# Kernel optimization log

Hardware: AMD Instinct MI355X
Metric: run time of the kernel (lower is better)

The kernel has to match this reference:

```python
import jax, jax.numpy as jnp
import numpy as np

B, LQ, C = 2, 12240, 256
NH, NL, NP = 8, 4, 4          # heads, levels, points
D = C // NH                   # head dim = 32
SHAPES = np.array([[96, 96], [48, 48], [24, 24], [12, 12]], dtype=np.int32)
LEN_IN = int((SHAPES[:, 0] * SHAPES[:, 1]).sum())  # 12240


def setup_inputs() -> dict:
    key = jax.random.key(0)
    ks = jax.random.split(key, 10)
    start = np.concatenate([[0], np.cumsum(SHAPES[:, 0] * SHAPES[:, 1])[:-1]]).astype(np.int32)
    return {
        "query": jax.random.normal(ks[0], (B, LQ, C), jnp.float32),
        "reference_points": jax.random.uniform(ks[1], (B, LQ, NL, 2), jnp.float32),
        "input_flatten": jax.random.normal(ks[2], (B, LEN_IN, C), jnp.float32),
        "input_spatial_shapes": jnp.asarray(SHAPES),
        "input_level_start_index": jnp.asarray(start),
        # params (sampling_offsets weight kept small so samples land near the reference point)
        "W_off": jax.random.normal(ks[3], (C, NH * NL * NP * 2), jnp.float32) * 0.01,
        "b_off": jax.random.normal(ks[4], (NH * NL * NP * 2,), jnp.float32) * 0.1,
        "W_attn": jax.random.normal(ks[5], (C, NH * NL * NP), jnp.float32) * 0.02,
        "b_attn": jnp.zeros((NH * NL * NP,), jnp.float32),
        "W_val": jax.random.normal(ks[6], (C, C), jnp.float32) * (1.0 / np.sqrt(C)),
        "b_val": jnp.zeros((C,), jnp.float32),
        "W_out": jax.random.normal(ks[7], (C, C), jnp.float32) * (1.0 / np.sqrt(C)),
        "b_out": jnp.zeros((C,), jnp.float32),
    }


def _bilinear_sample(v, loc):
    """grid_sample(align_corners=False, padding=zeros) equivalent.
    v:   (B, Hl, Wl, NH, D) level feature map per head
    loc: (B, Lq, NH, NP, 2) normalized sampling locations in [0,1]
    ->   (B, Lq, NH, NP, D)
    """
    _, Hl, Wl, _, _ = v.shape
    x = loc[..., 0] * Wl - 0.5
    y = loc[..., 1] * Hl - 0.5
    x0 = jnp.floor(x); y0 = jnp.floor(y)
    lx = x - x0;       ly = y - y0
    x0i = x0.astype(jnp.int32); y0i = y0.astype(jnp.int32)
    bi = jnp.arange(v.shape[0])[:, None, None, None]
    hi = jnp.arange(NH)[None, None, :, None]

    def gather(yi, xi):
        valid = (yi >= 0) & (yi < Hl) & (xi >= 0) & (xi < Wl)
        yc = jnp.clip(yi, 0, Hl - 1)
        xc = jnp.clip(xi, 0, Wl - 1)
        g = v[bi, yc, xc, hi]                       # (B,Lq,NH,NP,D)
        return g * valid[..., None].astype(v.dtype)

    w00 = (1 - lx) * (1 - ly); w01 = lx * (1 - ly)
    w10 = (1 - lx) * ly;       w11 = lx * ly
    return (gather(y0i, x0i) * w00[..., None] + gather(y0i, x0i + 1) * w01[..., None]
            + gather(y0i + 1, x0i) * w10[..., None] + gather(y0i + 1, x0i + 1) * w11[..., None])


def reference(query, reference_points, input_flatten, input_spatial_shapes,
              input_level_start_index, W_off, b_off, W_attn, b_attn,
              W_val, b_val, W_out, b_out):
    shapes = np.asarray(input_spatial_shapes)          # static level geometry
    starts = np.asarray(input_level_start_index)

    value = (input_flatten @ W_val + b_val).reshape(B, LEN_IN, NH, D)
    offsets = (query @ W_off + b_off).reshape(B, LQ, NH, NL, NP, 2)
    attn = (query @ W_attn + b_attn).reshape(B, LQ, NH, NL * NP)
    attn = jax.nn.softmax(attn, axis=-1).reshape(B, LQ, NH, NL, NP)

    # normalizer is (W_l, H_l) per level
    normalizer = jnp.stack([input_spatial_shapes[:, 1], input_spatial_shapes[:, 0]], -1).astype(query.dtype)
    loc = (reference_points[:, :, None, :, None, :]
           + offsets / normalizer[None, None, None, :, None, :])  # (B,Lq,NH,NL,NP,2)

    out = jnp.zeros((B, LQ, NH, D), query.dtype)
    for l in range(NL):
        Hl, Wl = int(shapes[l, 0]), int(shapes[l, 1])
        s = int(starts[l])
        v_l = value[:, s:s + Hl * Wl].reshape(B, Hl, Wl, NH, D)
        sampled = _bilinear_sample(v_l, loc[:, :, :, l])            # (B,Lq,NH,NP,D)
        out = out + jnp.einsum("bqhpd,bqhp->bqhd", sampled, attn[:, :, :, l])
    out = out.reshape(B, LQ, C)
    return out @ W_out + b_out
```

## Files before the change

### kernel.cpp

```cpp
#include <hip/hip_runtime.h>
#include <math.h>

#define B_    2
#define LQ_   12240
#define C_    256
#define NH_   8
#define NL_   4
#define NP_   4
#define LEN_IN_ 12240
#define MROWS (B_*LQ_)
#define MF_   (MROWS/16)
#define KF_   8
#define APLANE ((size_t)MROWS * C_)
#define NBLK  383

typedef __attribute__((ext_vector_type(8))) short short8v;
typedef __attribute__((ext_vector_type(4))) float f32x4;

__device__ __forceinline__ ushort f2bf_hi(float f) {
    uint u = __builtin_bit_cast(uint, f);
    uint r = (u + 0x7fffu + ((u >> 16) & 1u)) >> 16;
    return (ushort)r;
}
__device__ __forceinline__ float bf2f(ushort h) {
    uint u = ((uint)h) << 16;
    return __builtin_bit_cast(float, u);
}

#define U4_VAL  0
#define U4_OFF  8192
#define U4_ATT  16384
#define U4_UHI  20480
#define U4_ULO  28672
#define PACKB_TOTAL 294912

__global__ __launch_bounds__(256) void pack_w_kernel(
    const float* __restrict__ Wv, const float* __restrict__ Wo,
    const float* __restrict__ Wa, const float* __restrict__ Wu,
    ushort* __restrict__ packB)
{
    int gid = blockIdx.x * 256 + threadIdx.x;
    if (gid >= 28672) return;
    const float* W; ushort* hi; ushort* lo = nullptr; int N, rel;
    if (gid < 8192)       { W = Wv; hi = packB;          N = 256; rel = gid; }
    else if (gid < 16384) { W = Wo; hi = packB + 65536;  N = 256; rel = gid - 8192; }
    else if (gid < 20480) { W = Wa; hi = packB + 131072; N = 128; rel = gid - 16384; }
    else { W = Wu; hi = packB + 163840; lo = packB + 229376; N = 256; rel = gid - 20480; }

    const int lane = rel & 63;
    const int kf   = (rel >> 6) & 7;
    const int nf   = rel >> 9;
    const int row0 = kf * 32 + (lane >> 4) * 8;
    const int col  = nf * 16 + (lane & 15);

    union { ushort u16[8]; uint4 u4; } ch, cl;
#pragma unroll
    for (int j = 0; j < 8; ++j) {
        float x = W[(size_t)(row0 + j) * N + col];
        ushort h = f2bf_hi(x);
        ch.u16[j] = h;
        cl.u16[j] = f2bf_hi(x - bf2f(h));
    }
    *reinterpret_cast<uint4*>(hi + (size_t)rel * 8) = ch.u4;
    if (lo) *reinterpret_cast<uint4*>(lo + (size_t)rel * 8) = cl.u4;
}

__global__ __launch_bounds__(512) void gemm_value_kernel(
    const float* __restrict__ A, const ushort* __restrict__ packB,
    const float* __restrict__ bias, ushort* __restrict__ Cg)
{
    const int t = threadIdx.x, lane = t & 63, wid = t >> 6;
    const int rowBase = blockIdx.x * 64;

    __shared__ ushort Als[2048 * 8];

#pragma unroll
    for (int i = 0; i < 4; ++i) {
        int frag = i * 512 + t;
        int fl = frag & 63, kf = (frag >> 6) & 7, mf = frag >> 9;
        int row = min(rowBase + mf * 16 + (fl & 15), MROWS - 1);
        int k0 = kf * 32 + (fl >> 4) * 8;
        const float4* s = reinterpret_cast<const float4*>(A + (size_t)row * 256 + k0);
        float4 v0 = s[0], v1 = s[1];
        float vv[8] = { v0.x, v0.y, v0.z, v0.w, v1.x, v1.y, v1.z, v1.w };
        union { ushort u16[8]; uint4 u4; } hh;
#pragma unroll
        for (int j = 0; j < 8; ++j) hh.u16[j] = f2bf_hi(vv[j]);
        *reinterpret_cast<uint4*>(&Als[(size_t)frag * 8]) = hh.u4;
    }
    __syncthreads();

    const uint4* B4 = reinterpret_cast<const uint4*>(packB) + U4_VAL;
    const uint4* A4 = reinterpret_cast<const uint4*>(Als);
    const int wnf = wid * 2;

    f32x4 acc[4][2];
#pragma unroll
    for (int mi = 0; mi < 4; ++mi)
#pragma unroll
        for (int f = 0; f < 2; ++f) acc[mi][f] = (f32x4)0.0f;

#pragma unroll
    for (int kf = 0; kf < KF_; ++kf) {
        uint4 bh[2], ah[4];
#pragma unroll
        for (int f = 0; f < 2; ++f) bh[f] = B4[((wnf + f) * KF_ + kf) * 64 + lane];
#pragma unroll
        for (int mi = 0; mi < 4; ++mi) ah[mi] = A4[(mi * KF_ + kf) * 64 + lane];
#pragma unroll
        for (int mi = 0; mi < 4; ++mi) {
            short8v a = __builtin_bit_cast(short8v, ah[mi]);
#pragma unroll
            for (int f = 0; f < 2; ++f)
                acc[mi][f] = __builtin_amdgcn_mfma_f32_16x16x32_bf16(
                    a, __builtin_bit_cast(short8v, bh[f]), acc[mi][f], 0, 0, 0);
        }
    }

    const int colLane = lane & 15, rquad = lane >> 4;
#pragma unroll
    for (int f = 0; f < 2; ++f) {
        int col = (wnf + f) * 16 + colLane;
        float bv = bias[col];
#pragma unroll
        for (int mi = 0; mi < 4; ++mi)
#pragma unroll
            for (int e = 0; e < 4; ++e) {
                int row = rowBase + mi * 16 + rquad * 4 + e;
                if (row < MROWS) Cg[(size_t)row * 256 + col] = f2bf_hi(acc[mi][f][e] + bv);
            }
    }
}

__global__ __launch_bounds__(768) void gemm_query_kernel(
    const float* __restrict__ A, const ushort* __restrict__ packB,
    const float* __restrict__ b_off, const float* __restrict__ b_attn,
    float* __restrict__ offsb, float* __restrict__ attnb)
{
    const int t = threadIdx.x, lane = t & 63, wid = t >> 6;
    const int rowBase = blockIdx.x * 64;

    __shared__ ushort Als[2048 * 8];

#pragma unroll
    for (int i = 0; i < 3; ++i) {
        int frag = i * 768 + t;
        if (frag < 2048) {
            int fl = frag & 63, kf = (frag >> 6) & 7, mf = frag >> 9;
            int row = min(rowBase + mf * 16 + (fl & 15), MROWS - 1);
            int k0 = kf * 32 + (fl >> 4) * 8;
            const float4* s = reinterpret_cast<const float4*>(A + (size_t)row * 256 + k0);
            float4 v0 = s[0], v1 = s[1];
            float vv[8] = { v0.x, v0.y, v0.z, v0.w, v1.x, v1.y, v1.z, v1.w };
            union { ushort u16[8]; uint4 u4; } hh;
#pragma unroll
            for (int j = 0; j < 8; ++j) hh.u16[j] = f2bf_hi(vv[j]);
            *reinterpret_cast<uint4*>(&Als[(size_t)frag * 8]) = hh.u4;
        }
    }
    __syncthreads();

    const bool isAttn = wid >= 8;
    const int wnf = (isAttn ? (wid - 8) : wid) * 2;
    const uint4* B4 = reinterpret_cast<const uint4*>(packB) + (isAttn ? U4_ATT : U4_OFF);
    const uint4* A4 = reinterpret_cast<const uint4*>(Als);

    f32x4 acc[4][2];
#pragma unroll
    for (int mi = 0; mi < 4; ++mi)
#pragma unroll
        for (int f = 0; f < 2; ++f) acc[mi][f] = (f32x4)0.0f;

#pragma unroll
    for (int kf = 0; kf < KF_; ++kf) {
        uint4 bh[2], ah[4];
#pragma unroll
        for (int f = 0; f < 2; ++f) bh[f] = B4[((wnf + f) * KF_ + kf) * 64 + lane];
#pragma unroll
        for (int mi = 0; mi < 4; ++mi) ah[mi] = A4[(mi * KF_ + kf) * 64 + lane];
#pragma unroll
        for (int mi = 0; mi < 4; ++mi) {
            short8v a = __builtin_bit_cast(short8v, ah[mi]);
#pragma unroll
            for (int f = 0; f < 2; ++f)
                acc[mi][f] = __builtin_amdgcn_mfma_f32_16x16x32_bf16(
                    a, __builtin_bit_cast(short8v, bh[f]), acc[mi][f], 0, 0, 0);
        }
    }

    const int colLane = lane & 15, rquad = lane >> 4;
    const float* bias = isAttn ? b_attn : b_off;
    const int N = isAttn ? 128 : 256;
    float* outp = isAttn ? attnb : offsb;
#pragma unroll
    for (int f = 0; f < 2; ++f) {
        int col = (wnf + f) * 16 + colLane;
        float bv = bias[col];
#pragma unroll
        for (int mi = 0; mi < 4; ++mi)
#pragma unroll
            for (int e = 0; e < 4; ++e) {
                int row = rowBase + mi * 16 + rquad * 4 + e;
                if (row < MROWS) outp[(size_t)row * N + col] = acc[mi][f][e] + bv;
            }
    }
}

__global__ __launch_bounds__(512) void gemm_out_kernel(
    const ushort* __restrict__ midH, const ushort* __restrict__ midL,
    const ushort* __restrict__ packB, const float* __restrict__ bias,
    float* __restrict__ Cg)
{
    const int t = threadIdx.x, lane = t & 63, wid = t >> 6;
    const int rowBase = blockIdx.x * 64;

    __shared__ ushort Ahs[2048 * 8];
    __shared__ ushort Alo[2048 * 8];

    const uint4* H4 = reinterpret_cast<const uint4*>(midH);
    const uint4* L4 = reinterpret_cast<const uint4*>(midL);
#pragma unroll
    for (int i = 0; i < 4; ++i) {
        int frag = i * 512 + t;
        int fl = frag & 63, kf = (frag >> 6) & 7, mf = frag >> 9;
        int row = min(rowBase + mf * 16 + (fl & 15), MROWS - 1);
        int kq = kf * 4 + (fl >> 4);
        *reinterpret_cast<uint4*>(&Ahs[(size_t)frag * 8]) = H4[(size_t)row * 32 + kq];
        *reinterpret_cast<uint4*>(&Alo[(size_t)frag * 8]) = L4[(size_t)row * 32 + kq];
    }
    __syncthreads();

    const uint4* BH4 = reinterpret_cast<const uint4*>(packB) + U4_UHI;
    const uint4* BL4 = reinterpret_cast<const uint4*>(packB) + U4_ULO;
    const uint4* AH4 = reinterpret_cast<const uint4*>(Ahs);
    const uint4* AL4 = reinterpret_cast<const uint4*>(Alo);
    const int wnf = wid * 2;

    f32x4 acc[4][2];
#pragma unroll
    for (int mi = 0; mi < 4; ++mi)
#pragma unroll
        for (int f = 0; f < 2; ++f) acc[mi][f] = (f32x4)0.0f;

#pragma unroll 2
    for (int kf = 0; kf < KF_; ++kf) {
        uint4 bh[2], bl[2], ah[4], al[4];
#pragma unroll
        for (int f = 0; f < 2; ++f) {
            bh[f] = BH4[((wnf + f) * KF_ + kf) * 64 + lane];
            bl[f] = BL4[((wnf + f) * KF_ + kf) * 64 + lane];
        }
#pragma unroll
        for (int mi = 0; mi < 4; ++mi) {
            ah[mi] = AH4[(mi * KF_ + kf) * 64 + lane];
            al[mi] = AL4[(mi * KF_ + kf) * 64 + lane];
        }
#pragma unroll
        for (int mi = 0; mi < 4; ++mi) {
            short8v a  = __builtin_bit_cast(short8v, ah[mi]);
            short8v av = __builtin_bit_cast(short8v, al[mi]);
#pragma unroll
            for (int f = 0; f < 2; ++f) {
                short8v b = __builtin_bit_cast(short8v, bh[f]);
                acc[mi][f] = __builtin_amdgcn_mfma_f32_16x16x32_bf16(a, b, acc[mi][f], 0, 0, 0);
                acc[mi][f] = __builtin_amdgcn_mfma_f32_16x16x32_bf16(
                    a, __builtin_bit_cast(short8v, bl[f]), acc[mi][f], 0, 0, 0);
                acc[mi][f] = __builtin_amdgcn_mfma_f32_16x16x32_bf16(av, b, acc[mi][f], 0, 0, 0);
            }
        }
    }

    const int colLane = lane & 15, rquad = lane >> 4;
#pragma unroll
    for (int f = 0; f < 2; ++f) {
        int col = (wnf + f) * 16 + colLane;
        float bv = bias[col];
#pragma unroll
        for (int mi = 0; mi < 4; ++mi)
#pragma unroll
            for (int e = 0; e < 4; ++e) {
                int row = rowBase + mi * 16 + rquad * 4 + e;
                if (row < MROWS) Cg[(size_t)row * 256 + col] = acc[mi][f][e] + bv;
            }
    }
}

__global__ __launch_bounds__(128) void sampler_kernel(
    const ushort* __restrict__ value,
    const float* __restrict__ offs,
    const float* __restrict__ attnw,
    const float* __restrict__ refp,
    ushort* __restrict__ midH, ushort* __restrict__ midL)
{
    const int t  = threadIdx.x;
    const int qi = t >> 6;
    const int t6 = t & 63;
    const int q  = blockIdx.x * 2 + qi;

    __shared__ float s_ref[2][8];
    __shared__ int   s_addr[2][576];
    __shared__ float s_w[2][576];

    if (t < 16) s_ref[t >> 3][t & 7] = refp[(size_t)(blockIdx.x * 2 + (t >> 3)) * 8 + (t & 7)];
    __syncthreads();

#pragma unroll
    for (int batch = 0; batch < 2; ++batch) {
        const int p  = t6 + batch * 64;
        const int h  = p >> 4;
        const int lp = p & 15;
        const int l  = lp >> 2;

        float raw = attnw[(size_t)q * 128 + p];
        float mx = raw;
#pragma unroll
        for (int m = 8; m >= 1; m >>= 1) mx = fmaxf(mx, __shfl_xor(mx, m, 16));
        float e = __expf(raw - mx);
        float sum = e;
#pragma unroll
        for (int m = 8; m >= 1; m >>= 1) sum += __shfl_xor(sum, m, 16);
        const float aw = e / sum;

        const float2 o = reinterpret_cast<const float2*>(offs)[(size_t)q * 128 + p];
        const float rx = s_ref[qi][l * 2 + 0];
        const float ry = s_ref[qi][l * 2 + 1];

        const int   Wl = 96 >> l;
        const int   st = 12288 - (12288 >> (2 * l));
        const float fW = (float)Wl;

        const float x = fmaf(rx, fW, o.x) - 0.5f;
        const float y = fmaf(ry, fW, o.y) - 0.5f;
        const float x0f = floorf(x), y0f = floorf(y);
        const float fx = x - x0f, fy = y - y0f;
        const int x0 = (int)x0f, y0 = (int)y0f;
        const int x1 = x0 + 1,   y1 = y0 + 1;

        const float vx0 = (x0 >= 0 && x0 < Wl) ? 1.f : 0.f;
        const float vx1 = (x1 >= 0 && x1 < Wl) ? 1.f : 0.f;
        const float vy0 = (y0 >= 0 && y0 < Wl) ? 1.f : 0.f;
        const float vy1 = (y1 >= 0 && y1 < Wl) ? 1.f : 0.f;

        const int xc0 = min(max(x0, 0), Wl - 1);
        const int xc1 = min(max(x1, 0), Wl - 1);
        const int yc0 = min(max(y0, 0), Wl - 1);
        const int yc1 = min(max(y1, 0), Wl - 1);

        const int row0 = st + yc0 * Wl;
        const int row1 = st + yc1 * Wl;
        const int hb   = h << 5;

        const int sidx = (lp * 9 + h) * 4;
        int4 a;
        a.x = ((row0 + xc0) << 8) + hb;
        a.y = ((row0 + xc1) << 8) + hb;
        a.z = ((row1 + xc0) << 8) + hb;
        a.w = ((row1 + xc1) << 8) + hb;
        *reinterpret_cast<int4*>(&s_addr[qi][sidx]) = a;

        float4 w;
        w.x = aw * (1.f - fx) * (1.f - fy) * vx0 * vy0;
        w.y = aw * fx * (1.f - fy) * vx1 * vy0;
        w.z = aw * (1.f - fx) * fy * vx0 * vy1;
        w.w = aw * fx * fy * vx1 * vy1;
        *reinterpret_cast<float4*>(&s_w[qi][sidx]) = w;
    }
    __syncthreads();

    const int c2 = t6 >> 5;
    const int h  = (t6 >> 2) & 7;
    const int l2 = t6 & 3;
    const int d8 = l2 * 8;
    const ushort* __restrict__ vb = value + (q >= LQ_ ? (size_t)LEN_IN_ * 256 : 0) + d8;

    float acc[8];
#pragma unroll
    for (int j = 0; j < 8; ++j) acc[j] = 0.f;

#pragma unroll
    for (int pt = 0; pt < 16; ++pt) {
        const int base = (pt * 9 + h) * 4 + c2 * 2;
        const int2   a = *reinterpret_cast<const int2*>(&s_addr[qi][base]);
        const float2 w = *reinterpret_cast<const float2*>(&s_w[qi][base]);
        uint4 v0 = *reinterpret_cast<const uint4*>(vb + a.x);
        uint4 v1 = *reinterpret_cast<const uint4*>(vb + a.y);
        uint u;
#pragma unroll
        for (int j = 0; j < 4; ++j) {
            u = (&v0.x)[j];
            acc[2*j]   = fmaf(w.x, __builtin_bit_cast(float, u << 16), acc[2*j]);
            acc[2*j+1] = fmaf(w.x, __builtin_bit_cast(float, u), acc[2*j+1]);
        }
#pragma unroll
        for (int j = 0; j < 4; ++j) {
            u = (&v1.x)[j];
            acc[2*j]   = fmaf(w.y, __builtin_bit_cast(float, u << 16), acc[2*j]);
            acc[2*j+1] = fmaf(w.y, __builtin_bit_cast(float, u), acc[2*j+1]);
        }
    }

#pragma unroll
    for (int j = 0; j < 8; ++j) acc[j] += __shfl_xor(acc[j], 32);

    if (c2 == 0) {
        union { ushort u16[8]; uint4 u4; } hh, ll;
#pragma unroll
        for (int j = 0; j < 8; ++j) {
            ushort hb16 = f2bf_hi(acc[j]);
            hh.u16[j] = hb16;
            ll.u16[j] = f2bf_hi(acc[j] - bf2f(hb16));
        }
        const size_t base = (size_t)q * 256 + (h << 5) + d8;
        *reinterpret_cast<uint4*>(midH + base) = hh.u4;
        *reinterpret_cast<uint4*>(midL + base) = ll.u4;
    }
}

extern "C" void kernel_launch(void* const* d_in, const int* in_sizes, int n_in,
                              void* d_out, int out_size, void* d_ws, size_t ws_size,
                              hipStream_t stream)
{
    const float* query  = (const float*)d_in[0];
    const float* refp   = (const float*)d_in[1];
    const float* inflat = (const float*)d_in[2];
    const float* W_off  = (const float*)d_in[5];
    const float* b_off  = (const float*)d_in[6];
    const float* W_attn = (const float*)d_in[7];
    const float* b_attn = (const float*)d_in[8];
    const float* W_val  = (const float*)d_in[9];
    const float* b_val  = (const float*)d_in[10];
    const float* W_out  = (const float*)d_in[11];
    const float* b_out  = (const float*)d_in[12];
    float* out = (float*)d_out;

    ushort* midH  = (ushort*)d_ws;
    ushort* midL  = midH + APLANE;
    ushort* valbf = midL + APLANE;
    ushort* packB = valbf + APLANE;
    float*  offsb = (float*)(packB + PACKB_TOTAL);
    float*  attnb = offsb + APLANE;

    hipLaunchKernelGGL(pack_w_kernel, dim3(112), dim3(256), 0, stream,
                       W_val, W_off, W_attn, W_out, packB);
    hipLaunchKernelGGL(gemm_value_kernel, dim3(NBLK), dim3(512), 0, stream,
                       inflat, packB, b_val, valbf);
    hipLaunchKernelGGL(gemm_query_kernel, dim3(NBLK), dim3(768), 0, stream,
                       query, packB, b_off, b_attn, offsb, attnb);
    hipLaunchKernelGGL(sampler_kernel, dim3(MROWS / 2), dim3(128), 0, stream,
                       valbf, offsb, attnb, refp, midH, midL);
    hipLaunchKernelGGL(gemm_out_kernel, dim3(NBLK), dim3(512), 0, stream,
                       midH, midL, packB, b_out, out);
}
```

Baseline: 94.97 us.

## Merge value/query GEMMs, fuse softmax into GEMM, drop split-bf16 mid plane

Combines the value and query projection GEMMs into one launch with a 2D grid, and moves the attention softmax into the query GEMM epilogue via 16-lane shuffles. The sampler output is now stored as a single bf16 plane rather than a hi/lo pair, which removes a write and read of the residual plane and one MFMA per step in the output GEMM. The sampler inner loop uses packed 2-wide FMAs. This cuts a launch and memory traffic but lowers the precision of the intermediate sampled features.

```diff
diff --git a/kernel.cpp b/kernel.cpp
--- a/kernel.cpp
+++ b/kernel.cpp
@@ -16,6 +16,8 @@
 
 typedef __attribute__((ext_vector_type(8))) short short8v;
 typedef __attribute__((ext_vector_type(4))) float f32x4;
+typedef __attribute__((ext_vector_type(2))) float f32x2;
+typedef __attribute__((ext_vector_type(2))) uint  u32x2;
 
 __device__ __forceinline__ ushort f2bf_hi(float f) {
     uint u = __builtin_bit_cast(uint, f);
@@ -65,12 +67,17 @@
     if (lo) *reinterpret_cast<uint4*>(lo + (size_t)rel * 8) = cl.u4;
 }
 
-__global__ __launch_bounds__(512) void gemm_value_kernel(
-    const float* __restrict__ A, const ushort* __restrict__ packB,
-    const float* __restrict__ bias, ushort* __restrict__ Cg)
+__global__ __launch_bounds__(512) void gemm_vq_kernel(
+    const float* __restrict__ inflat, const float* __restrict__ query,
+    const ushort* __restrict__ packB,
+    const float* __restrict__ b_val, const float* __restrict__ b_off,
+    const float* __restrict__ b_attn,
+    ushort* __restrict__ valbf, float* __restrict__ offsb, float* __restrict__ attnb)
 {
     const int t = threadIdx.x, lane = t & 63, wid = t >> 6;
     const int rowBase = blockIdx.x * 64;
+    const bool isVal = (blockIdx.y == 0);
+    const float* __restrict__ A = isVal ? inflat : query;
 
     __shared__ ushort Als[2048 * 8];
 
@@ -90,135 +97,116 @@
     }
     __syncthreads();
 
-    const uint4* B4 = reinterpret_cast<const uint4*>(packB) + U4_VAL;
     const uint4* A4 = reinterpret_cast<const uint4*>(Als);
+    const int colLane = lane & 15, rquad = lane >> 4;
     const int wnf = wid * 2;
 
-    f32x4 acc[4][2];
-#pragma unroll
-    for (int mi = 0; mi < 4; ++mi)
-#pragma unroll
-        for (int f = 0; f < 2; ++f) acc[mi][f] = (f32x4)0.0f;
-
-#pragma unroll
-    for (int kf = 0; kf < KF_; ++kf) {
-        uint4 bh[2], ah[4];
-#pragma unroll
-        for (int f = 0; f < 2; ++f) bh[f] = B4[((wnf + f) * KF_ + kf) * 64 + lane];
-#pragma unroll
-        for (int mi = 0; mi < 4; ++mi) ah[mi] = A4[(mi * KF_ + kf) * 64 + lane];
-#pragma unroll
-        for (int mi = 0; mi < 4; ++mi) {
-            short8v a = __builtin_bit_cast(short8v, ah[mi]);
-#pragma unroll
-            for (int f = 0; f < 2; ++f)
-                acc[mi][f] = __builtin_amdgcn_mfma_f32_16x16x32_bf16(
-                    a, __builtin_bit_cast(short8v, bh[f]), acc[mi][f], 0, 0, 0);
-        }
-    }
-
-    const int colLane = lane & 15, rquad = lane >> 4;
-#pragma unroll
-    for (int f = 0; f < 2; ++f) {
-        int col = (wnf + f) * 16 + colLane;
-        float bv = bias[col];
+    if (isVal) {
+        const uint4* B4 = reinterpret_cast<const uint4*>(packB) + U4_VAL;
+        f32x4 acc[4][2];
 #pragma unroll
         for (int mi = 0; mi < 4; ++mi)
 #pragma unroll
-            for (int e = 0; e < 4; ++e) {
-                int row = rowBase + mi * 16 + rquad * 4 + e;
-                if (row < MROWS) Cg[(size_t)row * 256 + col] = f2bf_hi(acc[mi][f][e] + bv);
+            for (int f = 0; f < 2; ++f) acc[mi][f] = (f32x4)0.0f;
+
+#pragma unroll
+        for (int kf = 0; kf < KF_; ++kf) {
+            uint4 bh[2], ah[4];
+#pragma unroll
+            for (int f = 0; f < 2; ++f) bh[f] = B4[((wnf + f) * KF_ + kf) * 64 + lane];
+#pragma unroll
+            for (int mi = 0; mi < 4; ++mi) ah[mi] = A4[(mi * KF_ + kf) * 64 + lane];
+#pragma unroll
+            for (int mi = 0; mi < 4; ++mi) {
+                short8v a = __builtin_bit_cast(short8v, ah[mi]);
+#pragma unroll
+                for (int f = 0; f < 2; ++f)
+                    acc[mi][f] = __builtin_amdgcn_mfma_f32_16x16x32_bf16(
+                        a, __builtin_bit_cast(short8v, bh[f]), acc[mi][f], 0, 0, 0);
             }
-    }
-}
-
-__global__ __launch_bounds__(768) void gemm_query_kernel(
-    const float* __restrict__ A, const ushort* __restrict__ packB,
-    const float* __restrict__ b_off, const float* __restrict__ b_attn,
-    float* __restrict__ offsb, float* __restrict__ attnb)
+        }
+#pragma unroll
+        for (int f = 0; f < 2; ++f) {
+            int col = (wnf + f) * 16 + colLane;
+            float bv = b_val[col];
+#pragma unroll
+            for (int mi = 0; mi < 4; ++mi)
+#pragma unroll
+                for (int e = 0; e < 4; ++e) {
+                    int row = rowBase + mi * 16 + rquad * 4 + e;
+                    if (row < MROWS) valbf[(size_t)row * 256 + col] = f2bf_hi(acc[mi][f][e] + bv);
+                }
+        }
+    } else {
+        const uint4* BO = reinterpret_cast<const uint4*>(packB) + U4_OFF;
+        const uint4* BA = reinterpret_cast<const uint4*>(packB) + U4_ATT;
+        f32x4 acc[4][3];
+#pragma unroll
+        for (int mi = 0; mi < 4; ++mi)
+#pragma unroll
+            for (int f = 0; f < 3; ++f) acc[mi][f] = (f32x4)0.0f;
+
+#pragma unroll
+        for (int kf = 0; kf < KF_; ++kf) {
+            uint4 bh[3], ah[4];
+#pragma unroll
+            for (int f = 0; f < 2; ++f) bh[f] = BO[((wnf + f) * KF_ + kf) * 64 + lane];
+            bh[2] = BA[(wid * KF_ + kf) * 64 + lane];
+#pragma unroll
+            for (int mi = 0; mi < 4; ++mi) ah[mi] = A4[(mi * KF_ + kf) * 64 + lane];
+#pragma unroll
+            for (int mi = 0; mi < 4; ++mi) {
+                short8v a = __builtin_bit_cast(short8v, ah[mi]);
+#pragma unroll
+                for (int f = 0; f < 3; ++f)
+                    acc[mi][f] = __builtin_amdgcn_mfma_f32_16x16x32_bf16(
+                        a, __builtin_bit_cast(short8v, bh[f]), acc[mi][f], 0, 0, 0);
+            }
+        }
+#pragma unroll
+        for (int f = 0; f < 2; ++f) {
+            int col = (wnf + f) * 16 + colLane;
+            float bv = b_off[col];
+#pragma unroll
+            for (int mi = 0; mi < 4; ++mi)
+#pragma unroll
+                for (int e = 0; e < 4; ++e) {
+                    int row = rowBase + mi * 16 + rquad * 4 + e;
+                    if (row < MROWS) offsb[(size_t)row * 256 + col] = acc[mi][f][e] + bv;
+                }
+        }
+        {
+            int col = wid * 16 + colLane;
+            float bv = b_attn[col];
+#pragma unroll
+            for (int mi = 0; mi < 4; ++mi)
+#pragma unroll
+                for (int e = 0; e < 4; ++e) {
+                    float v = acc[mi][2][e] + bv;
+                    float mx = v;
+#pragma unroll
+                    for (int m = 8; m >= 1; m >>= 1) mx = fmaxf(mx, __shfl_xor(mx, m, 16));
+                    float ex = __expf(v - mx);
+                    float s = ex;
+#pragma unroll
+                    for (int m = 8; m >= 1; m >>= 1) s += __shfl_xor(s, m, 16);
+                    int row = rowBase + mi * 16 + rquad * 4 + e;
+                    if (row < MROWS) attnb[(size_t)row * 128 + col] = ex / s;
+                }
+        }
+    }
+}
+
+__global__ __launch_bounds__(512) void gemm_out_kernel(
+    const ushort* __restrict__ midH, const ushort* __restrict__ packB,
+    const float* __restrict__ bias, float* __restrict__ Cg)
 {
     const int t = threadIdx.x, lane = t & 63, wid = t >> 6;
     const int rowBase = blockIdx.x * 64;
 
-    __shared__ ushort Als[2048 * 8];
-
-#pragma unroll
-    for (int i = 0; i < 3; ++i) {
-        int frag = i * 768 + t;
-        if (frag < 2048) {
-            int fl = frag & 63, kf = (frag >> 6) & 7, mf = frag >> 9;
-            int row = min(rowBase + mf * 16 + (fl & 15), MROWS - 1);
-            int k0 = kf * 32 + (fl >> 4) * 8;
-            const float4* s = reinterpret_cast<const float4*>(A + (size_t)row * 256 + k0);
-            float4 v0 = s[0], v1 = s[1];
-            float vv[8] = { v0.x, v0.y, v0.z, v0.w, v1.x, v1.y, v1.z, v1.w };
-            union { ushort u16[8]; uint4 u4; } hh;
-#pragma unroll
-            for (int j = 0; j < 8; ++j) hh.u16[j] = f2bf_hi(vv[j]);
-            *reinterpret_cast<uint4*>(&Als[(size_t)frag * 8]) = hh.u4;
-        }
-    }
-    __syncthreads();
-
-    const bool isAttn = wid >= 8;
-    const int wnf = (isAttn ? (wid - 8) : wid) * 2;
-    const uint4* B4 = reinterpret_cast<const uint4*>(packB) + (isAttn ? U4_ATT : U4_OFF);
-    const uint4* A4 = reinterpret_cast<const uint4*>(Als);
-
-    f32x4 acc[4][2];
-#pragma unroll
-    for (int mi = 0; mi < 4; ++mi)
-#pragma unroll
-        for (int f = 0; f < 2; ++f) acc[mi][f] = (f32x4)0.0f;
-
-#pragma unroll
-    for (int kf = 0; kf < KF_; ++kf) {
-        uint4 bh[2], ah[4];
-#pragma unroll
-        for (int f = 0; f < 2; ++f) bh[f] = B4[((wnf + f) * KF_ + kf) * 64 + lane];
-#pragma unroll
-        for (int mi = 0; mi < 4; ++mi) ah[mi] = A4[(mi * KF_ + kf) * 64 + lane];
-#pragma unroll
-        for (int mi = 0; mi < 4; ++mi) {
-            short8v a = __builtin_bit_cast(short8v, ah[mi]);
-#pragma unroll
-            for (int f = 0; f < 2; ++f)
-                acc[mi][f] = __builtin_amdgcn_mfma_f32_16x16x32_bf16(
-                    a, __builtin_bit_cast(short8v, bh[f]), acc[mi][f], 0, 0, 0);
-        }
-    }
-
-    const int colLane = lane & 15, rquad = lane >> 4;
-    const float* bias = isAttn ? b_attn : b_off;
-    const int N = isAttn ? 128 : 256;
-    float* outp = isAttn ? attnb : offsb;
-#pragma unroll
-    for (int f = 0; f < 2; ++f) {
-        int col = (wnf + f) * 16 + colLane;
-        float bv = bias[col];
-#pragma unroll
-        for (int mi = 0; mi < 4; ++mi)
-#pragma unroll
-            for (int e = 0; e < 4; ++e) {
-                int row = rowBase + mi * 16 + rquad * 4 + e;
-                if (row < MROWS) outp[(size_t)row * N + col] = acc[mi][f][e] + bv;
-            }
-    }
-}
-
-__global__ __launch_bounds__(512) void gemm_out_kernel(
-    const ushort* __restrict__ midH, const ushort* __restrict__ midL,
-    const ushort* __restrict__ packB, const float* __restrict__ bias,
-    float* __restrict__ Cg)
-{
-    const int t = threadIdx.x, lane = t & 63, wid = t >> 6;
-    const int rowBase = blockIdx.x * 64;
-
     __shared__ ushort Ahs[2048 * 8];
-    __shared__ ushort Alo[2048 * 8];
 
     const uint4* H4 = reinterpret_cast<const uint4*>(midH);
-    const uint4* L4 = reinterpret_cast<const uint4*>(midL);
 #pragma unroll
     for (int i = 0; i < 4; ++i) {
         int frag = i * 512 + t;
@@ -226,14 +214,12 @@
         int row = min(rowBase + mf * 16 + (fl & 15), MROWS - 1);
         int kq = kf * 4 + (fl >> 4);
         *reinterpret_cast<uint4*>(&Ahs[(size_t)frag * 8]) = H4[(size_t)row * 32 + kq];
-        *reinterpret_cast<uint4*>(&Alo[(size_t)frag * 8]) = L4[(size_t)row * 32 + kq];
     }
     __syncthreads();
 
     const uint4* BH4 = reinterpret_cast<const uint4*>(packB) + U4_UHI;
     const uint4* BL4 = reinterpret_cast<const uint4*>(packB) + U4_ULO;
-    const uint4* AH4 = reinterpret_cast<const uint4*>(Ahs);
-    const uint4* AL4 = reinterpret_cast<const uint4*>(Alo);
+    const uint4* A4 = reinterpret_cast<const uint4*>(Ahs);
     const int wnf = wid * 2;
 
     f32x4 acc[4][2];
@@ -242,30 +228,25 @@
 #pragma unroll
         for (int f = 0; f < 2; ++f) acc[mi][f] = (f32x4)0.0f;
 
-#pragma unroll 2
+#pragma unroll
     for (int kf = 0; kf < KF_; ++kf) {
-        uint4 bh[2], bl[2], ah[4], al[4];
+        uint4 bh[2], bl[2], ah[4];
 #pragma unroll
         for (int f = 0; f < 2; ++f) {
             bh[f] = BH4[((wnf + f) * KF_ + kf) * 64 + lane];
             bl[f] = BL4[((wnf + f) * KF_ + kf) * 64 + lane];
         }
 #pragma unroll
+        for (int mi = 0; mi < 4; ++mi) ah[mi] = A4[(mi * KF_ + kf) * 64 + lane];
+#pragma unroll
         for (int mi = 0; mi < 4; ++mi) {
-            ah[mi] = AH4[(mi * KF_ + kf) * 64 + lane];
-            al[mi] = AL4[(mi * KF_ + kf) * 64 + lane];
-        }
-#pragma unroll
-        for (int mi = 0; mi < 4; ++mi) {
-            short8v a  = __builtin_bit_cast(short8v, ah[mi]);
-            short8v av = __builtin_bit_cast(short8v, al[mi]);
+            short8v a = __builtin_bit_cast(short8v, ah[mi]);
 #pragma unroll
             for (int f = 0; f < 2; ++f) {
-                short8v b = __builtin_bit_cast(short8v, bh[f]);
-                acc[mi][f] = __builtin_amdgcn_mfma_f32_16x16x32_bf16(a, b, acc[mi][f], 0, 0, 0);
+                acc[mi][f] = __builtin_amdgcn_mfma_f32_16x16x32_bf16(
+                    a, __builtin_bit_cast(short8v, bh[f]), acc[mi][f], 0, 0, 0);
                 acc[mi][f] = __builtin_amdgcn_mfma_f32_16x16x32_bf16(
                     a, __builtin_bit_cast(short8v, bl[f]), acc[mi][f], 0, 0, 0);
-                acc[mi][f] = __builtin_amdgcn_mfma_f32_16x16x32_bf16(av, b, acc[mi][f], 0, 0, 0);
             }
         }
     }
@@ -290,7 +271,7 @@
     const float* __restrict__ offs,
     const float* __restrict__ attnw,
     const float* __restrict__ refp,
-    ushort* __restrict__ midH, ushort* __restrict__ midL)
+    ushort* __restrict__ midH)
 {
     const int t  = threadIdx.x;
     const int qi = t >> 6;
@@ -311,16 +292,7 @@
         const int lp = p & 15;
         const int l  = lp >> 2;
 
-        float raw = attnw[(size_t)q * 128 + p];
-        float mx = raw;
-#pragma unroll
-        for (int m = 8; m >= 1; m >>= 1) mx = fmaxf(mx, __shfl_xor(mx, m, 16));
-        float e = __expf(raw - mx);
-        float sum = e;
-#pragma unroll
-        for (int m = 8; m >= 1; m >>= 1) sum += __shfl_xor(sum, m, 16);
-        const float aw = e / sum;
-
+        const float aw = attnw[(size_t)q * 128 + p];
         const float2 o = reinterpret_cast<const float2*>(offs)[(size_t)q * 128 + p];
         const float rx = s_ref[qi][l * 2 + 0];
         const float ry = s_ref[qi][l * 2 + 1];
@@ -373,9 +345,7 @@
     const int d8 = l2 * 8;
     const ushort* __restrict__ vb = value + (q >= LQ_ ? (size_t)LEN_IN_ * 256 : 0) + d8;
 
-    float acc[8];
-#pragma unroll
-    for (int j = 0; j < 8; ++j) acc[j] = 0.f;
+    f32x2 aLo = (f32x2)0.f, aHi = (f32x2)0.f, bLo = (f32x2)0.f, bHi = (f32x2)0.f;
 
 #pragma unroll
     for (int pt = 0; pt < 16; ++pt) {
@@ -384,35 +354,35 @@
         const float2 w = *reinterpret_cast<const float2*>(&s_w[qi][base]);
         uint4 v0 = *reinterpret_cast<const uint4*>(vb + a.x);
         uint4 v1 = *reinterpret_cast<const uint4*>(vb + a.y);
-        uint u;
-#pragma unroll
-        for (int j = 0; j < 4; ++j) {
-            u = (&v0.x)[j];
-            acc[2*j]   = fmaf(w.x, __builtin_bit_cast(float, u << 16), acc[2*j]);
-            acc[2*j+1] = fmaf(w.x, __builtin_bit_cast(float, u), acc[2*j+1]);
-        }
-#pragma unroll
-        for (int j = 0; j < 4; ++j) {
-            u = (&v1.x)[j];
-            acc[2*j]   = fmaf(w.y, __builtin_bit_cast(float, u << 16), acc[2*j]);
-            acc[2*j+1] = fmaf(w.y, __builtin_bit_cast(float, u), acc[2*j+1]);
-        }
-    }
-
-#pragma unroll
-    for (int j = 0; j < 8; ++j) acc[j] += __shfl_xor(acc[j], 32);
+        f32x2 w0; w0.x = w.x; w0.y = w.x;
+        f32x2 w1; w1.x = w.y; w1.y = w.y;
+
+        u32x2 h01; h01.x = v0.x; h01.y = v0.y;
+        u32x2 h23; h23.x = v0.z; h23.y = v0.w;
+        u32x2 l01 = h01 << 16, l23 = h23 << 16;
+        aHi = __builtin_elementwise_fma(__builtin_bit_cast(f32x2, h01), w0, aHi);
+        aLo = __builtin_elementwise_fma(__builtin_bit_cast(f32x2, l01), w0, aLo);
+        bHi = __builtin_elementwise_fma(__builtin_bit_cast(f32x2, h23), w0, bHi);
+        bLo = __builtin_elementwise_fma(__builtin_bit_cast(f32x2, l23), w0, bLo);
+
+        u32x2 g01; g01.x = v1.x; g01.y = v1.y;
+        u32x2 g23; g23.x = v1.z; g23.y = v1.w;
+        u32x2 m01 = g01 << 16, m23 = g23 << 16;
+        aHi = __builtin_elementwise_fma(__builtin_bit_cast(f32x2, g01), w1, aHi);
+        aLo = __builtin_elementwise_fma(__builtin_bit_cast(f32x2, m01), w1, aLo);
+        bHi = __builtin_elementwise_fma(__builtin_bit_cast(f32x2, g23), w1, bHi);
+        bLo = __builtin_elementwise_fma(__builtin_bit_cast(f32x2, m23), w1, bLo);
+    }
+
+    float r[8] = { aLo.x, aHi.x, aLo.y, aHi.y, bLo.x, bHi.x, bLo.y, bHi.y };
+#pragma unroll
+    for (int j = 0; j < 8; ++j) r[j] += __shfl_xor(r[j], 32);
 
     if (c2 == 0) {
-        union { ushort u16[8]; uint4 u4; } hh, ll;
-#pragma unroll
-        for (int j = 0; j < 8; ++j) {
-            ushort hb16 = f2bf_hi(acc[j]);
-            hh.u16[j] = hb16;
-            ll.u16[j] = f2bf_hi(acc[j] - bf2f(hb16));
-        }
-        const size_t base = (size_t)q * 256 + (h << 5) + d8;
-        *reinterpret_cast<uint4*>(midH + base) = hh.u4;
-        *reinterpret_cast<uint4*>(midL + base) = ll.u4;
+        union { ushort u16[8]; uint4 u4; } hh;
+#pragma unroll
+        for (int j = 0; j < 8; ++j) hh.u16[j] = f2bf_hi(r[j]);
+        *reinterpret_cast<uint4*>(midH + (size_t)q * 256 + (h << 5) + d8) = hh.u4;
     }
 }
 
@@ -434,20 +404,18 @@
     float* out = (float*)d_out;
 
     ushort* midH  = (ushort*)d_ws;
-    ushort* midL  = midH + APLANE;
-    ushort* valbf = midL + APLANE;
+    ushort* valbf = midH + APLANE;
     ushort* packB = valbf + APLANE;
     float*  offsb = (float*)(packB + PACKB_TOTAL);
     float*  attnb = offsb + APLANE;
 
     hipLaunchKernelGGL(pack_w_kernel, dim3(112), dim3(256), 0, stream,
                        W_val, W_off, W_attn, W_out, packB);
-    hipLaunchKernelGGL(gemm_value_kernel, dim3(NBLK), dim3(512), 0, stream,
-                       inflat, packB, b_val, valbf);
-    hipLaunchKernelGGL(gemm_query_kernel, dim3(NBLK), dim3(768), 0, stream,
-                       query, packB, b_off, b_attn, offsb, attnb);
+    hipLaunchKernelGGL(gemm_vq_kernel, dim3(NBLK, 2), dim3(512), 0, stream,
+                       inflat, query, packB, b_val, b_off, b_attn,
+                       valbf, offsb, attnb);
     hipLaunchKernelGGL(sampler_kernel, dim3(MROWS / 2), dim3(128), 0, stream,
-                       valbf, offsb, attnb, refp, midH, midL);
+                       valbf, offsb, attnb, refp, midH);
     hipLaunchKernelGGL(gemm_out_kernel, dim3(NBLK), dim3(512), 0, stream,
-                       midH, midL, packB, b_out, out);
-}
+                       midH, packB, b_out, out);
+}
```

New measurement: 89.20 us. 1.06x faster.
